# Kernel tuning notes

Hardware: AMD Instinct MI355X
Metric: run time of the kernel (lower is better)

Reference implementation:

```python
import jax, jax.numpy as jnp
import numpy as np

HIDDEN = 2048
NUM_HEADS = 16
NUM_KV_HEADS = 16
QK_NOPE = 128
QK_ROPE = 64
HEAD_DIM = QK_NOPE + QK_ROPE  # 192
V_HEAD = 128
KV_LORA = 512
Q_LORA = 1536
EPS = 1e-6


def rmsnorm(x, w):
    var = jnp.mean(x * x, axis=-1, keepdims=True)
    return x * jax.lax.rsqrt(var + EPS) * w


def setup_inputs() -> dict:
    key = jax.random.key(0)
    ks = jax.random.split(key, 8)
    s = lambda fan_in: 1.0 / np.sqrt(fan_in)
    return {
        "hidden_states": jax.random.normal(ks[0], (2, 2048, HIDDEN), jnp.float32),
        # weights stored as [in, out] so forward is x @ W
        "q_a_w": jax.random.normal(ks[1], (HIDDEN, Q_LORA), jnp.float32) * s(HIDDEN),
        "q_a_ln_w": jnp.ones((Q_LORA,), jnp.float32),
        "q_b_w": jax.random.normal(ks[2], (Q_LORA, NUM_HEADS * HEAD_DIM), jnp.float32) * s(Q_LORA),
        "kv_a_w": jax.random.normal(ks[3], (HIDDEN, KV_LORA + NUM_KV_HEADS * QK_ROPE), jnp.float32) * s(HIDDEN),
        "kv_a_ln_w": jnp.ones((KV_LORA,), jnp.float32),
        "kv_b_w": jax.random.normal(ks[4], (KV_LORA, NUM_KV_HEADS * (QK_NOPE + V_HEAD)), jnp.float32) * s(KV_LORA),
        "o_w": jax.random.normal(ks[5], (NUM_HEADS * V_HEAD, HIDDEN), jnp.float32) * s(NUM_HEADS * V_HEAD),
    }


def reference(hidden_states, q_a_w, q_a_ln_w, q_b_w, kv_a_w, kv_a_ln_w, kv_b_w, o_w):
    B, T, _ = hidden_states.shape
    # Q path: low-rank down-proj -> RMSNorm -> up-proj
    q = rmsnorm(hidden_states @ q_a_w, q_a_ln_w) @ q_b_w
    q = q.reshape(B, T, NUM_HEADS, HEAD_DIM)  # [B,T,H,192]

    # KV path: joint down-proj producing latent + rope slice
    kv_raw = hidden_states @ kv_a_w
    kv_latent = rmsnorm(kv_raw[..., :KV_LORA], kv_a_ln_w)
    k_rope = kv_raw[..., KV_LORA:].reshape(B, T, NUM_KV_HEADS, QK_ROPE)
    kv = (kv_latent @ kv_b_w).reshape(B, T, NUM_KV_HEADS, QK_NOPE + V_HEAD)
    k_nope = kv[..., :QK_NOPE]
    v = kv[..., QK_NOPE:]  # [B,T,Hkv,128]

    # NOTE: the original forward computes RoPE cos/sin but never applies the
    # rotation; q_rope/k_rope are used as-is (faithfully reproduced here).
    k = jnp.concatenate([k_nope, k_rope], axis=-1)  # [B,T,Hkv,192]
    # num_kv_groups == 1, so no repeat_interleave needed

    scale = 1.0 / jnp.sqrt(jnp.float32(HEAD_DIM))
    scores = jnp.einsum("bqhd,bkhd->bhqk", q, k) * scale  # [B,H,T,T]
    causal = jnp.tril(jnp.ones((T, T), bool))
    scores = jnp.where(causal, scores, jnp.finfo(scores.dtype).min)
    probs = jax.nn.softmax(scores, axis=-1)
    attn = jnp.einsum("bhqk,bkhd->bqhd", probs, v)  # [B,T,H,128]
    attn = attn.reshape(B, T, NUM_HEADS * V_HEAD)
    return attn @ o_w
```

## Files before the change

kernel.cpp:

```cpp
#include <hip/hip_runtime.h>
#include <cstdint>
#include <cstddef>

typedef unsigned short u16;
typedef short short8 __attribute__((ext_vector_type(8)));
typedef float f32x4 __attribute__((ext_vector_type(4)));

#define B_   2
#define T_   2048
#define H_   16
#define HID_ 2048
#define DQK_ 192
#define DV_  128
#define AW_  3072

__device__ __forceinline__ float bf2f(u16 u) {
  unsigned int v = ((unsigned int)u) << 16;
  return __builtin_bit_cast(float, v);
}
__device__ __forceinline__ u16 f2bf(float f) {
  unsigned int u = __builtin_bit_cast(unsigned int, f);
  u += 0x7fff + ((u >> 16) & 1);
  return (u16)(u >> 16);
}
__device__ __forceinline__ void load_lds16(const void* g, void* l) {
  __builtin_amdgcn_global_load_lds((const __attribute__((address_space(1))) void*)g,
                                   (__attribute__((address_space(3))) void*)l, 16, 0, 0);
}

__global__ __launch_bounds__(256) void cast_f32_bf16(const float* __restrict__ x,
                                                     u16* __restrict__ y) {
  size_t i = ((size_t)blockIdx.x * 256 + threadIdx.x) * 8;
  float4 a = *(const float4*)&x[i];
  float4 b = *(const float4*)&x[i + 4];
  u16 r[8];
  r[0] = f2bf(a.x); r[1] = f2bf(a.y); r[2] = f2bf(a.z); r[3] = f2bf(a.w);
  r[4] = f2bf(b.x); r[5] = f2bf(b.y); r[6] = f2bf(b.z); r[7] = f2bf(b.w);
  *(uint4*)&y[i] = *(const uint4*)&r[0];
}

__global__ __launch_bounds__(256) void transpose_cast_k(const float* __restrict__ W,
                                                        u16* __restrict__ Wt,
                                                        int K, int N) {
  __shared__ u16 tile[32][33];
  int n0 = blockIdx.x * 32, k0 = blockIdx.y * 32;
  int tx = threadIdx.x & 31, ty = threadIdx.x >> 5;
#pragma unroll
  for (int i = 0; i < 32; i += 8)
    tile[ty + i][tx] = f2bf(W[(size_t)(k0 + ty + i) * N + n0 + tx]);
  __syncthreads();
#pragma unroll
  for (int i = 0; i < 32; i += 8)
    Wt[(size_t)(n0 + ty + i) * K + k0 + tx] = tile[tx][ty + i];
}

__global__ __launch_bounds__(256) void rmsnorm_k(const u16* __restrict__ in, int in_stride,
                                                 int L, const float* __restrict__ w,
                                                 u16* __restrict__ out, int out_stride) {
  int row = blockIdx.x;
  const u16* x = in + (size_t)row * in_stride;
  float ss = 0.f;
  for (int i = threadIdx.x * 8; i < L; i += 2048) {
    uint4 v = *(const uint4*)&x[i];
    const u16* p = (const u16*)&v;
#pragma unroll
    for (int e = 0; e < 8; ++e) { float f = bf2f(p[e]); ss += f * f; }
  }
#pragma unroll
  for (int m = 32; m >= 1; m >>= 1) ss += __shfl_xor(ss, m);
  __shared__ float red[4];
  if ((threadIdx.x & 63) == 0) red[threadIdx.x >> 6] = ss;
  __syncthreads();
  ss = red[0] + red[1] + red[2] + red[3];
  float inv = rsqrtf(ss / (float)L + 1e-6f);
  u16* o = out + (size_t)row * out_stride;
  for (int i = threadIdx.x * 8; i < L; i += 2048) {
    uint4 v = *(const uint4*)&x[i];
    const u16* p = (const u16*)&v;
    u16 r8[8];
#pragma unroll
    for (int e = 0; e < 8; ++e) r8[e] = f2bf(bf2f(p[e]) * inv * w[i + e]);
    *(uint4*)&o[i] = *(const uint4*)&r8[0];
  }
}

template <int EPI>
__global__ __launch_bounds__(512) void gemm256(const u16* __restrict__ A,
                                               const u16* __restrict__ Bt,
                                               void* __restrict__ Cout,
                                               int M, int N, int K) {
  __shared__ u16 As[2][256 * 64];
  __shared__ u16 Bs[2][256 * 64];
  const int nbx = N >> 8;
  const int bx = blockIdx.x % nbx, by = blockIdx.x / nbx;
  const int m0 = by << 8, n0 = bx << 8;
  const int tid = threadIdx.x, w = tid >> 6, lane = tid & 63;
  const int wm = w >> 2, wn = w & 3;
  const int llo = lane & 15, lhi = lane >> 4;
  f32x4 acc[8][4] = {};

  const u16* srcp[8];
  int dsto[8];
#pragma unroll
  for (int jl = 0; jl < 2; ++jl) {
    int c = jl * 512 + tid;
    int i = c >> 3, sl = c & 7;
    { int r = ((i >> 6) << 7) + (i & 63);
      srcp[jl] = A + (size_t)(m0 + r) * K + ((sl ^ (r & 7)) << 3);
      dsto[jl] = (r * 8 + sl) * 8; }
    { int r = ((i >> 5) << 6) + (i & 31);
      srcp[2 + jl] = Bt + (size_t)(n0 + r) * K + ((sl ^ (r & 7)) << 3);
      dsto[2 + jl] = (r * 8 + sl) * 8; }
    { int r = ((i >> 5) << 6) + 32 + (i & 31);
      srcp[4 + jl] = Bt + (size_t)(n0 + r) * K + ((sl ^ (r & 7)) << 3);
      dsto[4 + jl] = (r * 8 + sl) * 8; }
    { int r = ((i >> 6) << 7) + 64 + (i & 63);
      srcp[6 + jl] = A + (size_t)(m0 + r) * K + ((sl ^ (r & 7)) << 3);
      dsto[6 + jl] = (r * 8 + sl) * 8; }
  }
#define STG(j, kt, buf)                                                        \
  load_lds16(srcp[j] + (size_t)(kt) * 64,                                      \
             ((j) < 2 || (j) >= 6) ? &As[(buf)][dsto[j]] : &Bs[(buf)][dsto[j]])

  auto rdA = [&](int buf, int mi, int ks) {
    int r = wm * 128 + mi * 16 + llo;
    return *(const short8*)&As[buf][r * 64 + (((ks * 4 + lhi) ^ (r & 7)) << 3)];
  };
  auto rdB = [&](int buf, int nj, int ks) {
    int r = wn * 64 + nj * 16 + llo;
    return *(const short8*)&Bs[buf][r * 64 + (((ks * 4 + lhi) ^ (r & 7)) << 3)];
  };

  const int NT = K >> 6;
#pragma unroll
  for (int j = 0; j < 8; ++j) STG(j, 0, 0);

  short8 af[4][2], bf[2][2];
  for (int kt = 0; kt < NT; ++kt) {
    const int cur = kt & 1, nxt = cur ^ 1;
    const bool hn = (kt + 1 < NT);
    asm volatile("s_waitcnt vmcnt(4)" ::: "memory");
    __builtin_amdgcn_s_barrier();
#pragma unroll
    for (int mi = 0; mi < 4; ++mi) { af[mi][0] = rdA(cur, mi, 0); af[mi][1] = rdA(cur, mi, 1); }
#pragma unroll
    for (int nj = 0; nj < 2; ++nj) { bf[nj][0] = rdB(cur, nj, 0); bf[nj][1] = rdB(cur, nj, 1); }
    if (hn) { STG(0, kt + 1, nxt); STG(1, kt + 1, nxt); }
    __builtin_amdgcn_s_setprio(1);
#pragma unroll
    for (int mi = 0; mi < 4; ++mi)
#pragma unroll
      for (int nj = 0; nj < 2; ++nj)
#pragma unroll
        for (int ks = 0; ks < 2; ++ks)
          acc[mi][nj] = __builtin_amdgcn_mfma_f32_16x16x32_bf16(af[mi][ks], bf[nj][ks], acc[mi][nj], 0, 0, 0);
    __builtin_amdgcn_s_setprio(0);
    if (hn) asm volatile("s_waitcnt vmcnt(4)" ::: "memory");
    else    asm volatile("s_waitcnt vmcnt(2)" ::: "memory");
    __builtin_amdgcn_s_barrier();
#pragma unroll
    for (int nj = 0; nj < 2; ++nj) { bf[nj][0] = rdB(cur, 2 + nj, 0); bf[nj][1] = rdB(cur, 2 + nj, 1); }
    if (hn) { STG(2, kt + 1, nxt); STG(3, kt + 1, nxt); }
    __builtin_amdgcn_s_setprio(1);
#pragma unroll
    for (int mi = 0; mi < 4; ++mi)
#pragma unroll
      for (int nj = 0; nj < 2; ++nj)
#pragma unroll
        for (int ks = 0; ks < 2; ++ks)
          acc[mi][2 + nj] = __builtin_amdgcn_mfma_f32_16x16x32_bf16(af[mi][ks], bf[nj][ks], acc[mi][2 + nj], 0, 0, 0);
    __builtin_amdgcn_s_setprio(0);
    if (hn) asm volatile("s_waitcnt vmcnt(4)" ::: "memory");
    else    asm volatile("s_waitcnt vmcnt(0)" ::: "memory");
    __builtin_amdgcn_s_barrier();
#pragma unroll
    for (int mi = 0; mi < 4; ++mi) { af[mi][0] = rdA(cur, 4 + mi, 0); af[mi][1] = rdA(cur, 4 + mi, 1); }
    if (hn) { STG(4, kt + 1, nxt); STG(5, kt + 1, nxt); }
    __builtin_amdgcn_s_setprio(1);
#pragma unroll
    for (int mi = 0; mi < 4; ++mi)
#pragma unroll
      for (int nj = 0; nj < 2; ++nj)
#pragma unroll
        for (int ks = 0; ks < 2; ++ks)
          acc[4 + mi][2 + nj] = __builtin_amdgcn_mfma_f32_16x16x32_bf16(af[mi][ks], bf[nj][ks], acc[4 + mi][2 + nj], 0, 0, 0);
    __builtin_amdgcn_s_setprio(0);
#pragma unroll
    for (int nj = 0; nj < 2; ++nj) { bf[nj][0] = rdB(cur, nj, 0); bf[nj][1] = rdB(cur, nj, 1); }
    if (hn) { STG(6, kt + 1, nxt); STG(7, kt + 1, nxt); }
    __builtin_amdgcn_s_setprio(1);
#pragma unroll
    for (int mi = 0; mi < 4; ++mi)
#pragma unroll
      for (int nj = 0; nj < 2; ++nj)
#pragma unroll
        for (int ks = 0; ks < 2; ++ks)
          acc[4 + mi][nj] = __builtin_amdgcn_mfma_f32_16x16x32_bf16(af[mi][ks], bf[nj][ks], acc[4 + mi][nj], 0, 0, 0);
    __builtin_amdgcn_s_setprio(0);
  }
#undef STG

  const float scale = (EPI == 3) ? 0.10412163f : 1.0f;
  u16* C = (u16*)Cout;
#pragma unroll
  for (int mi = 0; mi < 8; ++mi)
#pragma unroll
    for (int nj = 0; nj < 4; ++nj)
#pragma unroll
      for (int r = 0; r < 4; ++r)
        C[(size_t)(m0 + wm * 128 + mi * 16 + lhi * 4 + r) * N + (n0 + wn * 64 + nj * 16 + llo)] =
            f2bf(acc[mi][nj][r] * scale);
}

template <int EPI>
__global__ __launch_bounds__(256) void gemm_bt(const u16* __restrict__ A,
                                               const u16* __restrict__ Bt,
                                               void* __restrict__ Cout,
                                               int M, int N, int K) {
  __shared__ u16 As[3][128 * 32];
  __shared__ u16 Bs[3][128 * 32];
  const int nbx = N >> 7;
  const int bx = blockIdx.x % nbx, by = blockIdx.x / nbx;
  const int m0 = by << 7, n0 = bx << 7;
  const int tid = threadIdx.x, w = tid >> 6, lane = tid & 63;
  const int wr = w >> 1, wc = w & 1;
  const int llo = lane & 15, lhi = lane >> 4;
  f32x4 acc[4][4] = {};

  const int c0 = tid, c1 = tid + 256;
  const int ar0 = c0 >> 2, s0_ = c0 & 3;
  const int ar1 = c1 >> 2, s1_ = c1 & 3;
  const u16* Asrc0 = A + (size_t)(m0 + ar0) * K + (s0_ ^ ((ar0 >> 1) & 3)) * 8;
  const u16* Asrc1 = A + (size_t)(m0 + ar1) * K + (s1_ ^ ((ar1 >> 1) & 3)) * 8;
  const u16* Bsrc0 = Bt + (size_t)(n0 + ar0) * K + (s0_ ^ ((ar0 >> 1) & 3)) * 8;
  const u16* Bsrc1 = Bt + (size_t)(n0 + ar1) * K + (s1_ ^ ((ar1 >> 1) & 3)) * 8;

  int aoff[4], boff[4];
#pragma unroll
  for (int i = 0; i < 4; ++i) {
    int rowa = wr * 64 + i * 16 + llo;
    aoff[i] = (rowa * 4 + (lhi ^ ((rowa >> 1) & 3))) * 8;
    int rowb = wc * 64 + i * 16 + llo;
    boff[i] = (rowb * 4 + (lhi ^ ((rowb >> 1) & 3))) * 8;
  }

#define STAGE_KT(kt, buf)                                   \
  do {                                                      \
    int k0_ = (kt) << 5;                                    \
    load_lds16(Asrc0 + k0_, &As[(buf)][c0 * 8]);            \
    load_lds16(Asrc1 + k0_, &As[(buf)][c1 * 8]);            \
    load_lds16(Bsrc0 + k0_, &Bs[(buf)][c0 * 8]);            \
    load_lds16(Bsrc1 + k0_, &Bs[(buf)][c1 * 8]);            \
  } while (0)

  const int NT = K >> 5;
  STAGE_KT(0, 0);
  STAGE_KT(1, 1);
  asm volatile("s_waitcnt vmcnt(4)" ::: "memory");
  __builtin_amdgcn_s_barrier();

  int cur = 0, nxt = 2;
  for (int kt = 0; kt < NT; ++kt) {
    if (kt + 2 < NT) STAGE_KT(kt + 2, nxt);
    short8 af[4], bfr[4];
#pragma unroll
    for (int i = 0; i < 4; ++i) af[i] = *(const short8*)&As[cur][aoff[i]];
#pragma unroll
    for (int j = 0; j < 4; ++j) bfr[j] = *(const short8*)&Bs[cur][boff[j]];
    __builtin_amdgcn_s_setprio(1);
#pragma unroll
    for (int i = 0; i < 4; ++i)
#pragma unroll
      for (int j = 0; j < 4; ++j)
        acc[i][j] = __builtin_amdgcn_mfma_f32_16x16x32_bf16(af[i], bfr[j], acc[i][j], 0, 0, 0);
    __builtin_amdgcn_s_setprio(0);
    if (kt + 2 < NT) asm volatile("s_waitcnt vmcnt(4)" ::: "memory");
    else             asm volatile("s_waitcnt vmcnt(0)" ::: "memory");
    __builtin_amdgcn_s_barrier();
    cur = (cur == 2) ? 0 : cur + 1;
    nxt = (nxt == 2) ? 0 : nxt + 1;
  }
#undef STAGE_KT

  if constexpr (EPI == 0) {
    float* C = (float*)Cout;
#pragma unroll
    for (int i = 0; i < 4; ++i)
#pragma unroll
      for (int j = 0; j < 4; ++j)
#pragma unroll
        for (int r = 0; r < 4; ++r)
          C[(size_t)(m0 + wr * 64 + i * 16 + lhi * 4 + r) * N + (n0 + wc * 64 + j * 16 + llo)] =
              acc[i][j][r];
  } else {
    const float scale = (EPI == 3) ? 0.10412163f : 1.0f;
    u16* C = (u16*)Cout;
#pragma unroll
    for (int i = 0; i < 4; ++i)
#pragma unroll
      for (int j = 0; j < 4; ++j)
#pragma unroll
        for (int r = 0; r < 4; ++r)
          C[(size_t)(m0 + wr * 64 + i * 16 + lhi * 4 + r) * N + (n0 + wc * 64 + j * 16 + llo)] =
              f2bf(acc[i][j][r] * scale);
  }
}

__global__ __launch_bounds__(256) void pack_vt_k(const u16* __restrict__ kv, u16* __restrict__ Vt) {
  __shared__ u16 tile[64][136];
  const int nt = T_ / 64;
  int t0 = (blockIdx.x % nt) * 64;
  int bh = blockIdx.x / nt;
  int b = bh >> 4, h = bh & 15;
  int row = threadIdx.x >> 4;
  int ck = threadIdx.x & 15;
#pragma unroll
  for (int i = 0; i < 64; i += 16) {
    uint4 v = *(const uint4*)&kv[((size_t)(b * T_) + t0 + row + i) * 4096 + h * 256 + 128 + ck * 8];
    *(uint4*)&tile[row + i][ck * 8] = v;
  }
  __syncthreads();
  int d = threadIdx.x >> 1;
  int th = (threadIdx.x & 1) * 32;
  u16 tmp[32];
#pragma unroll
  for (int e = 0; e < 32; ++e) tmp[e] = tile[th + e][d];
#pragma unroll
  for (int e = 0; e < 32; e += 8)
    *(uint4*)&Vt[((size_t)bh * 128 + d) * T_ + t0 + th + e] = *(const uint4*)&tmp[e];
}

__global__ __launch_bounds__(256, 2) void attn_k(const u16* __restrict__ q,
                                                 const u16* __restrict__ kv,
                                                 const u16* __restrict__ kvraw,
                                                 const u16* __restrict__ Vt,
                                                 u16* __restrict__ att) {
  constexpr int KLD = 192, VLD = 64, PLD = 64;
  __shared__ u16 Ks[2][64 * KLD];
  __shared__ u16 Vs[128 * VLD];
  __shared__ u16 Ps[64 * PLD];
  const int p = (int)blockIdx.x;
  const int xcd = p & 7, j = p >> 3;
  const int bh = xcd * 4 + (j & 3);
  const int pr = j >> 2;
  const int b = bh >> 4, h = bh & 15;
  const int bT = b * T_;
  const int tid = threadIdx.x, w = tid >> 6, lane = tid & 63;
  const int llo = lane & 15, lhi = lane >> 4;
  const u16* Vb = Vt + (size_t)bh * DV_ * T_;

  const u16* kbase[6]; int kstr[6];
#pragma unroll
  for (int ii = 0; ii < 6; ++ii) {
    int c = ii * 256 + tid;
    int rr = c / 24, chk = c - rr * 24;
    int sc = chk ^ (rr & 7);
    if (sc < 16) { kbase[ii] = kv + (size_t)(bT + rr) * 4096 + h * 256 + sc * 8; kstr[ii] = 4096; }
    else { kbase[ii] = kvraw + (size_t)(bT + rr) * AW_ + 2048 + h * 64 + (sc - 16) * 8; kstr[ii] = AW_; }
  }
  int voff[4];
#pragma unroll
  for (int ii = 0; ii < 4; ++ii) {
    int c = ii * 256 + tid;
    int rr = c >> 3, chk = c & 7;
    voff[ii] = rr * T_ + (chk ^ (rr & 7)) * 8;
  }

#pragma unroll
  for (int pass = 0; pass < 2; ++pass) {
    const int qt = pass == 0 ? 31 - pr : pr;
    const int q0 = qt * 64;
    const int rbase = q0 + w * 16;
    short8 qf[6];
#pragma unroll
    for (int kk = 0; kk < 6; ++kk)
      qf[kk] = *(const short8*)&q[(size_t)(bT + rbase + llo) * AW_ + h * DQK_ + kk * 32 + lhi * 8];
    f32x4 oacc[8] = {};
    float m_r[4], l_r[4];
#pragma unroll
    for (int r = 0; r < 4; ++r) { m_r[r] = -1e30f; l_r[r] = 0.f; }

#pragma unroll
    for (int ii = 0; ii < 6; ++ii)
      load_lds16(kbase[ii], &Ks[0][(ii * 256 + tid) * 8]);
    asm volatile("s_waitcnt vmcnt(0)" ::: "memory");
    __builtin_amdgcn_s_barrier();
    __builtin_amdgcn_sched_barrier(0);

    const int nkt = qt + 1;
    int cur = 0;
    for (int kt = 0; kt < nkt; ++kt) {
      const int k0 = kt * 64;
      const bool hasNext = (kt + 1 < nkt);
#pragma unroll
      for (int ii = 0; ii < 4; ++ii)
        load_lds16(Vb + k0 + voff[ii], &Vs[(ii * 256 + tid) * 8]);
      if (hasNext) {
        u16* kd = Ks[cur ^ 1];
#pragma unroll
        for (int ii = 0; ii < 6; ++ii)
          load_lds16(kbase[ii] + (size_t)(k0 + 64) * kstr[ii], &kd[(ii * 256 + tid) * 8]);
      }
      const u16* kbuf = Ks[cur];
      f32x4 s[4] = {};
      __builtin_amdgcn_s_setprio(1);
#pragma unroll
      for (int kk = 0; kk < 6; ++kk) {
        const int col = kk * 32 + lhi * 8;
        short8 kf[4];
#pragma unroll
        for (int j2 = 0; j2 < 4; ++j2) {
          const int row = j2 * 16 + llo;
          kf[j2] = *(const short8*)&kbuf[row * KLD + (col ^ ((row & 7) << 3))];
        }
#pragma unroll
        for (int j2 = 0; j2 < 4; ++j2)
          s[j2] = __builtin_amdgcn_mfma_f32_16x16x32_bf16(qf[kk], kf[j2], s[j2], 0, 0, 0);
      }
      __builtin_amdgcn_s_setprio(0);
      const bool needMask = (k0 + 63 > rbase);
#pragma unroll
      for (int r = 0; r < 4; ++r) {
        const int qrow = rbase + lhi * 4 + r;
        float sv[4];
#pragma unroll
        for (int j2 = 0; j2 < 4; ++j2) {
          float x = s[j2][r];
          if (needMask) { int kcol = k0 + j2 * 16 + llo; x = (kcol <= qrow) ? x : -1e30f; }
          sv[j2] = x;
        }
        float mx4 = fmaxf(fmaxf(sv[0], sv[1]), fmaxf(sv[2], sv[3]));
        if (!__all(mx4 - m_r[r] <= 8.f)) {
          float mx = mx4;
#pragma unroll
          for (int mk = 1; mk < 16; mk <<= 1) mx = fmaxf(mx, __shfl_xor(mx, mk));
          float mnew = fmaxf(m_r[r], mx);
          float alpha = exp2f(m_r[r] - mnew);
          m_r[r] = mnew;
          l_r[r] *= alpha;
#pragma unroll
          for (int jo = 0; jo < 8; ++jo) oacc[jo][r] *= alpha;
        }
        float rs = 0.f;
        const int prow = w * 16 + lhi * 4 + r;
#pragma unroll
        for (int j2 = 0; j2 < 4; ++j2) {
          float p2 = exp2f(sv[j2] - m_r[r]);
          rs += p2;
          int pcol = j2 * 16 + llo;
          Ps[prow * PLD + (pcol ^ ((prow & 7) << 3))] = f2bf(p2);
        }
        l_r[r] += rs;
      }
      if (hasNext) asm volatile("s_waitcnt vmcnt(6)" ::: "memory");
      else         asm volatile("s_waitcnt vmcnt(0)" ::: "memory");
      __builtin_amdgcn_s_barrier();
      __builtin_amdgcn_sched_barrier(0);
      __builtin_amdgcn_s_setprio(1);
#pragma unroll
      for (int kk2 = 0; kk2 < 2; ++kk2) {
        const int prow = w * 16 + llo;
        const int pcol = kk2 * 32 + lhi * 8;
        short8 pf = *(const short8*)&Ps[prow * PLD + (pcol ^ ((prow & 7) << 3))];
#pragma unroll
        for (int jo = 0; jo < 8; ++jo) {
          const int vrow = jo * 16 + llo;
          short8 vf = *(const short8*)&Vs[vrow * VLD + (pcol ^ ((vrow & 7) << 3))];
          oacc[jo] = __builtin_amdgcn_mfma_f32_16x16x32_bf16(pf, vf, oacc[jo], 0, 0, 0);
        }
      }
      __builtin_amdgcn_s_setprio(0);
      asm volatile("s_waitcnt vmcnt(0)" ::: "memory");
      __builtin_amdgcn_s_barrier();
      __builtin_amdgcn_sched_barrier(0);
      cur ^= 1;
    }
#pragma unroll
    for (int r = 0; r < 4; ++r) {
      float lr = l_r[r];
#pragma unroll
      for (int mk = 1; mk < 16; mk <<= 1) lr += __shfl_xor(lr, mk);
      const int qrow = rbase + lhi * 4 + r;
      const float linv = 1.f / lr;
#pragma unroll
      for (int jo = 0; jo < 8; ++jo)
        att[((size_t)bT + qrow) * (H_ * DV_) + h * DV_ + jo * 16 + llo] =
            f2bf(oacc[jo][r] * linv);
    }
  }
}

extern "C" void kernel_launch(void* const* d_in, const int* in_sizes, int n_in,
                              void* d_out, int out_size, void* d_ws, size_t ws_size,
                              hipStream_t stream) {
  const float* hs      = (const float*)d_in[0];
  const float* q_a_w   = (const float*)d_in[1];
  const float* q_a_ln  = (const float*)d_in[2];
  const float* q_b_w   = (const float*)d_in[3];
  const float* kv_a_w  = (const float*)d_in[4];
  const float* kv_a_ln = (const float*)d_in[5];
  const float* kv_b_w  = (const float*)d_in[6];
  const float* o_w     = (const float*)d_in[7];
  float* out = (float*)d_out;
  char* ws = (char*)d_ws;

  u16* hid  = (u16*)(ws + 0);
  u16* wt   = (u16*)(ws + 16777216);
  u16* qa   = (u16*)(ws + 29360128);
  u16* qan  = (u16*)(ws + 54525952);
  u16* qout = (u16*)(ws + 67108864);
  u16* att  = (u16*)(ws + 92274688);
  u16* kv   = (u16*)(ws + 109051904);
  u16* Vt   = (u16*)(ws + 142606336);

  cast_f32_bf16<<<4096, 256, 0, stream>>>(hs, hid);

  transpose_cast_k<<<dim3(1536 / 32, 2048 / 32), 256, 0, stream>>>(q_a_w, wt, 2048, 1536);
  transpose_cast_k<<<dim3(1536 / 32, 2048 / 32), 256, 0, stream>>>(kv_a_w, wt + (size_t)1536 * 2048, 2048, 1536);
  gemm256<1><<<(3072 / 256) * (4096 / 256), 512, 0, stream>>>(hid, wt, qa, 4096, 3072, 2048);

  rmsnorm_k<<<4096, 256, 0, stream>>>(qa, AW_, 1536, q_a_ln, qan, 1536);

  transpose_cast_k<<<dim3(3072 / 32, 1536 / 32), 256, 0, stream>>>(q_b_w, wt, 1536, 3072);
  gemm256<3><<<(3072 / 256) * (4096 / 256), 512, 0, stream>>>(qan, wt, qout, 4096, 3072, 1536);

  rmsnorm_k<<<4096, 256, 0, stream>>>(qa + 1536, AW_, 512, kv_a_ln, qan, 512);

  transpose_cast_k<<<dim3(4096 / 32, 512 / 32), 256, 0, stream>>>(kv_b_w, wt, 512, 4096);
  gemm256<1><<<(4096 / 256) * (4096 / 256), 512, 0, stream>>>(qan, wt, kv, 4096, 4096, 512);

  pack_vt_k<<<1024, 256, 0, stream>>>(kv, Vt);

  attn_k<<<512, 256, 0, stream>>>(qout, kv, qa, Vt, att);

  transpose_cast_k<<<dim3(2048 / 32, 2048 / 32), 256, 0, stream>>>(o_w, wt, 2048, 2048);
  gemm_bt<0><<<(2048 / 128) * (4096 / 128), 256, 0, stream>>>(att, wt, out, 4096, 2048, 2048);
}
```

Baseline: 320.7 us.

## Fuse V-transpose into kv GEMM epilogue and merge both RMSNorms

The separate pack_vt kernel is removed. The kv up-projection GEMM epilogue (EPI==2) now writes the V half directly in transposed [bh,d,T] layout alongside the normal output. The two RMSNorm launches are merged into one kernel that writes to two separate buffers, and the attention loop strength-reduces its K/V pointer arithmetic. This saves two launches and one read-back of the kv buffer, at the cost of strided 8-byte transposed stores in the GEMM epilogue.

```diff
diff --git a/kernel.cpp b/kernel.cpp
--- a/kernel.cpp
+++ b/kernel.cpp
@@ -54,33 +54,63 @@
     Wt[(size_t)(n0 + ty + i) * K + k0 + tx] = tile[tx][ty + i];
 }
 
-__global__ __launch_bounds__(256) void rmsnorm_k(const u16* __restrict__ in, int in_stride,
-                                                 int L, const float* __restrict__ w,
-                                                 u16* __restrict__ out, int out_stride) {
-  int row = blockIdx.x;
-  const u16* x = in + (size_t)row * in_stride;
-  float ss = 0.f;
-  for (int i = threadIdx.x * 8; i < L; i += 2048) {
-    uint4 v = *(const uint4*)&x[i];
-    const u16* p = (const u16*)&v;
-#pragma unroll
-    for (int e = 0; e < 8; ++e) { float f = bf2f(p[e]); ss += f * f; }
-  }
-#pragma unroll
-  for (int m = 32; m >= 1; m >>= 1) ss += __shfl_xor(ss, m);
+__global__ __launch_bounds__(256) void rmsnorm_dual(const u16* __restrict__ qa,
+                                                    const float* __restrict__ w1,
+                                                    u16* __restrict__ out1,
+                                                    const float* __restrict__ w2,
+                                                    u16* __restrict__ out2) {
   __shared__ float red[4];
-  if ((threadIdx.x & 63) == 0) red[threadIdx.x >> 6] = ss;
+  const int row = blockIdx.x, tid = threadIdx.x;
+  {
+    const u16* x = qa + (size_t)row * AW_;
+    float ss = 0.f;
+    for (int i = tid * 8; i < 1536; i += 2048) {
+      uint4 v = *(const uint4*)&x[i];
+      const u16* p = (const u16*)&v;
+#pragma unroll
+      for (int e = 0; e < 8; ++e) { float f = bf2f(p[e]); ss += f * f; }
+    }
+#pragma unroll
+    for (int m = 32; m >= 1; m >>= 1) ss += __shfl_xor(ss, m);
+    if ((tid & 63) == 0) red[tid >> 6] = ss;
+    __syncthreads();
+    ss = red[0] + red[1] + red[2] + red[3];
+    float inv = rsqrtf(ss / 1536.f + 1e-6f);
+    u16* o = out1 + (size_t)row * 1536;
+    for (int i = tid * 8; i < 1536; i += 2048) {
+      uint4 v = *(const uint4*)&x[i];
+      const u16* p = (const u16*)&v;
+      u16 r8[8];
+#pragma unroll
+      for (int e = 0; e < 8; ++e) r8[e] = f2bf(bf2f(p[e]) * inv * w1[i + e]);
+      *(uint4*)&o[i] = *(const uint4*)&r8[0];
+    }
+  }
   __syncthreads();
-  ss = red[0] + red[1] + red[2] + red[3];
-  float inv = rsqrtf(ss / (float)L + 1e-6f);
-  u16* o = out + (size_t)row * out_stride;
-  for (int i = threadIdx.x * 8; i < L; i += 2048) {
-    uint4 v = *(const uint4*)&x[i];
-    const u16* p = (const u16*)&v;
-    u16 r8[8];
-#pragma unroll
-    for (int e = 0; e < 8; ++e) r8[e] = f2bf(bf2f(p[e]) * inv * w[i + e]);
-    *(uint4*)&o[i] = *(const uint4*)&r8[0];
+  {
+    const u16* x = qa + (size_t)row * AW_ + 1536;
+    float ss = 0.f;
+    for (int i = tid * 8; i < 512; i += 2048) {
+      uint4 v = *(const uint4*)&x[i];
+      const u16* p = (const u16*)&v;
+#pragma unroll
+      for (int e = 0; e < 8; ++e) { float f = bf2f(p[e]); ss += f * f; }
+    }
+#pragma unroll
+    for (int m = 32; m >= 1; m >>= 1) ss += __shfl_xor(ss, m);
+    if ((tid & 63) == 0) red[tid >> 6] = ss;
+    __syncthreads();
+    ss = red[0] + red[1] + red[2] + red[3];
+    float inv = rsqrtf(ss / 512.f + 1e-6f);
+    u16* o = out2 + (size_t)row * 512;
+    for (int i = tid * 8; i < 512; i += 2048) {
+      uint4 v = *(const uint4*)&x[i];
+      const u16* p = (const u16*)&v;
+      u16 r8[8];
+#pragma unroll
+      for (int e = 0; e < 8; ++e) r8[e] = f2bf(bf2f(p[e]) * inv * w2[i + e]);
+      *(uint4*)&o[i] = *(const uint4*)&r8[0];
+    }
   }
 }
 
@@ -88,6 +118,7 @@
 __global__ __launch_bounds__(512) void gemm256(const u16* __restrict__ A,
                                                const u16* __restrict__ Bt,
                                                void* __restrict__ Cout,
+                                               u16* __restrict__ Vt2,
                                                int M, int N, int K) {
   __shared__ u16 As[2][256 * 64];
   __shared__ u16 Bs[2][256 * 64];
@@ -205,11 +236,25 @@
 #pragma unroll
   for (int mi = 0; mi < 8; ++mi)
 #pragma unroll
-    for (int nj = 0; nj < 4; ++nj)
-#pragma unroll
-      for (int r = 0; r < 4; ++r)
+    for (int nj = 0; nj < 4; ++nj) {
+      u16 vals[4];
+#pragma unroll
+      for (int r = 0; r < 4; ++r) {
+        vals[r] = f2bf(acc[mi][nj][r] * scale);
         C[(size_t)(m0 + wm * 128 + mi * 16 + lhi * 4 + r) * N + (n0 + wn * 64 + nj * 16 + llo)] =
-            f2bf(acc[mi][nj][r] * scale);
+            vals[r];
+      }
+      if constexpr (EPI == 2) {
+        if (wn >= 2) {
+          const int n = n0 + wn * 64 + nj * 16 + llo;
+          const int mb = m0 + wm * 128 + mi * 16 + lhi * 4;
+          const int bb = mb >> 11, t = mb & 2047;
+          const int h = n >> 8, d = (n & 255) - 128;
+          *(uint2*)&Vt2[((size_t)((bb << 4) + h) * 128 + d) * (size_t)T_ + t] =
+              *(const uint2*)&vals[0];
+        }
+      }
+    }
 }
 
 template <int EPI>
@@ -293,7 +338,6 @@
           C[(size_t)(m0 + wr * 64 + i * 16 + lhi * 4 + r) * N + (n0 + wc * 64 + j * 16 + llo)] =
               acc[i][j][r];
   } else {
-    const float scale = (EPI == 3) ? 0.10412163f : 1.0f;
     u16* C = (u16*)Cout;
 #pragma unroll
     for (int i = 0; i < 4; ++i)
@@ -302,32 +346,8 @@
 #pragma unroll
         for (int r = 0; r < 4; ++r)
           C[(size_t)(m0 + wr * 64 + i * 16 + lhi * 4 + r) * N + (n0 + wc * 64 + j * 16 + llo)] =
-              f2bf(acc[i][j][r] * scale);
-  }
-}
-
-__global__ __launch_bounds__(256) void pack_vt_k(const u16* __restrict__ kv, u16* __restrict__ Vt) {
-  __shared__ u16 tile[64][136];
-  const int nt = T_ / 64;
-  int t0 = (blockIdx.x % nt) * 64;
-  int bh = blockIdx.x / nt;
-  int b = bh >> 4, h = bh & 15;
-  int row = threadIdx.x >> 4;
-  int ck = threadIdx.x & 15;
-#pragma unroll
-  for (int i = 0; i < 64; i += 16) {
-    uint4 v = *(const uint4*)&kv[((size_t)(b * T_) + t0 + row + i) * 4096 + h * 256 + 128 + ck * 8];
-    *(uint4*)&tile[row + i][ck * 8] = v;
-  }
-  __syncthreads();
-  int d = threadIdx.x >> 1;
-  int th = (threadIdx.x & 1) * 32;
-  u16 tmp[32];
-#pragma unroll
-  for (int e = 0; e < 32; ++e) tmp[e] = tile[th + e][d];
-#pragma unroll
-  for (int e = 0; e < 32; e += 8)
-    *(uint4*)&Vt[((size_t)bh * 128 + d) * T_ + t0 + th + e] = *(const uint4*)&tmp[e];
+              f2bf(acc[i][j][r]);
+  }
 }
 
 __global__ __launch_bounds__(256, 2) void attn_k(const u16* __restrict__ q,
@@ -387,6 +407,13 @@
     __builtin_amdgcn_s_barrier();
     __builtin_amdgcn_sched_barrier(0);
 
+    const u16* kp[6];
+#pragma unroll
+    for (int ii = 0; ii < 6; ++ii) kp[ii] = kbase[ii] + (size_t)64 * kstr[ii];
+    const u16* vp[4];
+#pragma unroll
+    for (int ii = 0; ii < 4; ++ii) vp[ii] = Vb + voff[ii];
+
     const int nkt = qt + 1;
     int cur = 0;
     for (int kt = 0; kt < nkt; ++kt) {
@@ -394,13 +421,17 @@
       const bool hasNext = (kt + 1 < nkt);
 #pragma unroll
       for (int ii = 0; ii < 4; ++ii)
-        load_lds16(Vb + k0 + voff[ii], &Vs[(ii * 256 + tid) * 8]);
+        load_lds16(vp[ii], &Vs[(ii * 256 + tid) * 8]);
       if (hasNext) {
         u16* kd = Ks[cur ^ 1];
 #pragma unroll
         for (int ii = 0; ii < 6; ++ii)
-          load_lds16(kbase[ii] + (size_t)(k0 + 64) * kstr[ii], &kd[(ii * 256 + tid) * 8]);
+          load_lds16(kp[ii], &kd[(ii * 256 + tid) * 8]);
       }
+#pragma unroll
+      for (int ii = 0; ii < 4; ++ii) vp[ii] += 64;
+#pragma unroll
+      for (int ii = 0; ii < 6; ++ii) kp[ii] += (size_t)64 * kstr[ii];
       const u16* kbuf = Ks[cur];
       f32x4 s[4] = {};
       __builtin_amdgcn_s_setprio(1);
@@ -512,24 +543,21 @@
   u16* att  = (u16*)(ws + 92274688);
   u16* kv   = (u16*)(ws + 109051904);
   u16* Vt   = (u16*)(ws + 142606336);
+  u16* qan2 = (u16*)(ws + 159383552);
 
   cast_f32_bf16<<<4096, 256, 0, stream>>>(hs, hid);
 
   transpose_cast_k<<<dim3(1536 / 32, 2048 / 32), 256, 0, stream>>>(q_a_w, wt, 2048, 1536);
   transpose_cast_k<<<dim3(1536 / 32, 2048 / 32), 256, 0, stream>>>(kv_a_w, wt + (size_t)1536 * 2048, 2048, 1536);
-  gemm256<1><<<(3072 / 256) * (4096 / 256), 512, 0, stream>>>(hid, wt, qa, 4096, 3072, 2048);
-
-  rmsnorm_k<<<4096, 256, 0, stream>>>(qa, AW_, 1536, q_a_ln, qan, 1536);
+  gemm256<1><<<(3072 / 256) * (4096 / 256), 512, 0, stream>>>(hid, wt, qa, nullptr, 4096, 3072, 2048);
+
+  rmsnorm_dual<<<4096, 256, 0, stream>>>(qa, q_a_ln, qan, kv_a_ln, qan2);
 
   transpose_cast_k<<<dim3(3072 / 32, 1536 / 32), 256, 0, stream>>>(q_b_w, wt, 1536, 3072);
-  gemm256<3><<<(3072 / 256) * (4096 / 256), 512, 0, stream>>>(qan, wt, qout, 4096, 3072, 1536);
-
-  rmsnorm_k<<<4096, 256, 0, stream>>>(qa + 1536, AW_, 512, kv_a_ln, qan, 512);
+  gemm256<3><<<(3072 / 256) * (4096 / 256), 512, 0, stream>>>(qan, wt, qout, nullptr, 4096, 3072, 1536);
 
   transpose_cast_k<<<dim3(4096 / 32, 512 / 32), 256, 0, stream>>>(kv_b_w, wt, 512, 4096);
-  gemm256<1><<<(4096 / 256) * (4096 / 256), 512, 0, stream>>>(qan, wt, kv, 4096, 4096, 512);
-
-  pack_vt_k<<<1024, 256, 0, stream>>>(kv, Vt);
+  gemm256<2><<<(4096 / 256) * (4096 / 256), 512, 0, stream>>>(qan2, wt, kv, Vt, 4096, 4096, 512);
 
   attn_k<<<512, 256, 0, stream>>>(qout, kv, qa, Vt, att);
 
```

After: 315.5 us. No clear change (-1.6%).
